# Kernel tuning notes

Measured on AMD Instinct MI355X. Metric: run time of the kernel, lower is better.

Reference implementation:

```python
import jax, jax.numpy as jnp
import numpy as np

N_NODES = 100000
LATENT_DIM = 8
SAMPLE_SIZE = 8192
N_EDGES = 1000000
EPS = 1e-6


def setup_inputs() -> dict:
    key = jax.random.key(0)
    k1, k2, k3, k4, k5 = jax.random.split(key, 5)
    latent_Z = jax.random.normal(k1, (N_NODES, LATENT_DIM), dtype=jnp.float32)
    alpha = jax.random.normal(k2, (1,), dtype=jnp.float32)
    sample_idx = jax.random.randint(k3, (SAMPLE_SIZE,), 0, N_NODES, dtype=jnp.int64)
    sparse_sample_i = jax.random.randint(k4, (N_EDGES,), 0, N_NODES, dtype=jnp.int64)
    sparse_sample_j = jax.random.randint(k5, (N_EDGES,), 0, N_NODES, dtype=jnp.int64)
    return {"latent_Z": latent_Z, "alpha": alpha, "sample_idx": sample_idx,
            "sparse_sample_i": sparse_sample_i, "sparse_sample_j": sparse_sample_j}


def reference(latent_Z, alpha, sample_idx, sparse_sample_i, sparse_sample_j):
    # --- dense non-edge term over the sampled subgraph ---
    Zs = latent_Z[sample_idx]                              # [S, D]
    diff = Zs[:, None, :] - Zs[None, :, :] + EPS           # [S, S, D]
    dist = jnp.sqrt(jnp.sum(diff * diff, axis=-1))         # [S, S]
    mat = jnp.exp(-dist)                                   # [S, S]
    # original uses exp(ones) vectors in the matmul-with-ones trick -> factor e^2
    ones_exp_sq = jnp.exp(jnp.float32(1.0)) ** 2
    offdiag_sum = jnp.sum(mat) - jnp.sum(jnp.diagonal(mat))
    z_pdist1 = jnp.exp(alpha[0]) * 0.5 * ones_exp_sq * offdiag_sum
    # --- sparse positive-edge term ---
    ed = latent_Z[sparse_sample_i] - latent_Z[sparse_sample_j] + EPS  # [E, D]
    edist = jnp.sqrt(jnp.sum(ed * ed, axis=-1))                        # [E]
    z_pdist2 = jnp.sum(-edist + alpha[0])
    return z_pdist2 - z_pdist1
```

## Files before the change

kernel.cpp:

```cpp
#include <hip/hip_runtime.h>
#include <hip/hip_bf16.h>
#include <math.h>

#define NNODES   100000
#define S        8192
#define D        8
#define EPSF     1e-6f
#define LOG2E    1.442695040888963f
#define EPS_S    (LOG2E * EPSF)
#define NT2      256

#define ZHL_OFF  0
#define U_OFF    262144
#define V_OFF    294912
#define DP_OFF   327680
#define SP_OFF   331776
#define ZB_OFF   332800

#define NSBLK    256
#define NDBLK    1024
#define NWPP     32

typedef __attribute__((ext_vector_type(8)))  short short8_t;
typedef __attribute__((ext_vector_type(16))) float f32x16;

__device__ __forceinline__ float block_reduce_f(float v, float* sm) {
    #pragma unroll
    for (int off = 32; off > 0; off >>= 1) v += __shfl_down(v, off, 64);
    int lane = threadIdx.x & 63, wid = threadIdx.x >> 6;
    if (lane == 0) sm[wid] = v;
    __syncthreads();
    float s = 0.f;
    if (threadIdx.x == 0) {
        for (int w = 0; w < 4; ++w) s += sm[w];
    }
    return s;
}

__global__ __launch_bounds__(256) void gather_kernel(const float* __restrict__ Z,
                                                     const int* __restrict__ idx,
                                                     ushort* __restrict__ zhl,
                                                     float* __restrict__ u,
                                                     float* __restrict__ v,
                                                     ushort* __restrict__ zb16) {
    int gid = blockIdx.x * 256 + threadIdx.x;

    if (gid < S) {
        int n = idx[gid];
        const float4* zp = (const float4*)(Z + (size_t)n * D);
        float4 a = zp[0], b = zp[1];
        float z[8] = { a.x, a.y, a.z, a.w, b.x, b.y, b.z, b.w };
        float ss = 0.f;
        short8_t h, l;
        #pragma unroll
        for (int k = 0; k < 8; ++k) {
            float zs = LOG2E * z[k];
            ss = fmaf(zs, zs, ss);
            __hip_bfloat16 hb = __float2bfloat16(zs);
            float hf = __bfloat162float(hb);
            __hip_bfloat16 lb = __float2bfloat16(zs - hf);
            h[k] = (short)__builtin_bit_cast(unsigned short, hb);
            l[k] = (short)__builtin_bit_cast(unsigned short, lb);
        }
        *(short8_t*)(zhl + (size_t)gid * 16)     = h;
        *(short8_t*)(zhl + (size_t)gid * 16 + 8) = l;
        u[gid] = ss + 8.f * EPS_S * EPS_S;
        v[gid] = ss;
    }

    if (gid < NNODES) {
        const float4* zp = (const float4*)(Z + (size_t)gid * D);
        float4 a = zp[0], b = zp[1];
        float z[8] = { a.x, a.y, a.z, a.w, b.x, b.y, b.z, b.w };
        short8_t o;
        #pragma unroll
        for (int k = 0; k < 8; ++k) {
            __hip_bfloat16 bb = __float2bfloat16(z[k]);
            o[k] = (short)__builtin_bit_cast(unsigned short, bb);
        }
        *(short8_t*)(zb16 + (size_t)gid * 8) = o;
    }
}

#define UNPACK8(u4, f)                                        \
    f[0] = __uint_as_float(u4.x << 16);                       \
    f[1] = __uint_as_float(u4.x & 0xffff0000u);               \
    f[2] = __uint_as_float(u4.y << 16);                       \
    f[3] = __uint_as_float(u4.y & 0xffff0000u);               \
    f[4] = __uint_as_float(u4.z << 16);                       \
    f[5] = __uint_as_float(u4.z & 0xffff0000u);               \
    f[6] = __uint_as_float(u4.w << 16);                       \
    f[7] = __uint_as_float(u4.w & 0xffff0000u);

__device__ __forceinline__ float edge_dist4(const uint4* __restrict__ zb,
                                            int4 ia, int4 ib) {
    float acc = 0.f;
    int aidx[4] = { ia.x, ia.y, ia.z, ia.w };
    int bidx[4] = { ib.x, ib.y, ib.z, ib.w };
    #pragma unroll
    for (int q = 0; q < 4; ++q) {
        uint4 ua = zb[aidx[q]];
        uint4 ub = zb[bidx[q]];
        float fa[8], fb[8];
        UNPACK8(ua, fa);
        UNPACK8(ub, fb);
        float s2 = 0.f;
        #pragma unroll
        for (int k = 0; k < 8; ++k) {
            float d = fa[k] - fb[k] + EPSF;
            s2 = fmaf(d, d, s2);
        }
        acc += __builtin_amdgcn_sqrtf(s2);
    }
    return acc;
}

__device__ __forceinline__ void dense_sweep32(const ushort* __restrict__ zhl,
                                              const float* __restrict__ v,
                                              short8_t afrag, const float4* u4,
                                              int ti, int tj0, int cnt, int c31,
                                              float& ax, float& ay, float& az, float& aw) {
    const ushort* bp = zhl + (size_t)(tj0 * 32 + c31) * 16;
    const float*  vp = v + tj0 * 32 + c31;
    short8_t bh = *(const short8_t*)bp;
    short8_t bl = *(const short8_t*)(bp + 8);
    float    vt = vp[0];
    #pragma unroll 2
    for (int t = 0; t < cnt; ++t) {
        short8_t bhc = bh, blc = bl;
        float    vtc = vt;
        if (t + 1 < cnt) {
            bh = *(const short8_t*)(bp + (size_t)(t + 1) * 512);
            bl = *(const short8_t*)(bp + (size_t)(t + 1) * 512 + 8);
            vt = vp[(t + 1) * 32];
        }
        float w = (tj0 + t == ti) ? 1.f : 2.f;
        f32x16 c = { 0.f, 0.f, 0.f, 0.f, 0.f, 0.f, 0.f, 0.f,
                     0.f, 0.f, 0.f, 0.f, 0.f, 0.f, 0.f, 0.f };
        c = __builtin_amdgcn_mfma_f32_32x32x16_bf16(afrag, bhc, c, 0, 0, 0);
        c = __builtin_amdgcn_mfma_f32_32x32x16_bf16(afrag, blc, c, 0, 0, 0);
        #pragma unroll
        for (int q = 0; q < 4; ++q) {
            float s0 = u4[q].x + vtc, s1 = u4[q].y + vtc;
            float s2 = u4[q].z + vtc, s3 = u4[q].w + vtc;
            float d0 = fmaf(c[4*q+0], -2.f, s0);
            float d1 = fmaf(c[4*q+1], -2.f, s1);
            float d2 = fmaf(c[4*q+2], -2.f, s2);
            float d3 = fmaf(c[4*q+3], -2.f, s3);
            ax = fmaf(w, __builtin_amdgcn_exp2f(-__builtin_amdgcn_sqrtf(__builtin_fabsf(d0))), ax);
            ay = fmaf(w, __builtin_amdgcn_exp2f(-__builtin_amdgcn_sqrtf(__builtin_fabsf(d1))), ay);
            az = fmaf(w, __builtin_amdgcn_exp2f(-__builtin_amdgcn_sqrtf(__builtin_fabsf(d2))), az);
            aw = fmaf(w, __builtin_amdgcn_exp2f(-__builtin_amdgcn_sqrtf(__builtin_fabsf(d3))), aw);
        }
    }
}

__global__ __launch_bounds__(256) void fused_kernel(
        const ushort* __restrict__ zhl, const float* __restrict__ u,
        const float* __restrict__ v, const ushort* __restrict__ zb16,
        const int* __restrict__ ei, const int* __restrict__ ej, int ne,
        float* __restrict__ dpart, float* __restrict__ spart) {
    __shared__ float red[4];
    int tid = threadIdx.x, bx = blockIdx.x;

    if (bx < NSBLK) {
        const uint4* zb = (const uint4*)zb16;
        float acc = 0.f;
        int nchunk = ne >> 2;
        int stride = NSBLK * 256;
        int c = bx * 256 + tid;
        if (c < nchunk) {
            int4 ia = ((const int4*)ei)[c];
            int4 ib = ((const int4*)ej)[c];
            while (true) {
                int cn = c + stride;
                int4 ian, ibn;
                bool more = cn < nchunk;
                if (more) {
                    ian = ((const int4*)ei)[cn];
                    ibn = ((const int4*)ej)[cn];
                }
                acc += edge_dist4(zb, ia, ib);
                if (!more) break;
                ia = ian; ib = ibn; c = cn;
            }
        }
        for (int e = (nchunk << 2) + bx * 256 + tid; e < ne; e += stride) {
            uint4 ua = zb[ei[e]];
            uint4 ub = zb[ej[e]];
            float fa[8], fb[8];
            UNPACK8(ua, fa);
            UNPACK8(ub, fb);
            float s2 = 0.f;
            #pragma unroll
            for (int k = 0; k < 8; ++k) {
                float d = fa[k] - fb[k] + EPSF;
                s2 = fmaf(d, d, s2);
            }
            acc += __builtin_amdgcn_sqrtf(s2);
        }
        float s = block_reduce_f(acc, red);
        if (tid == 0) spart[bx] = s;
        return;
    }

    int dbx  = bx - NSBLK;
    int wave = tid >> 6, lane = tid & 63;
    int g = lane >> 5, c31 = lane & 31;

    int p  = dbx >> 3;
    int wv = (dbx & 7) * 4 + wave;
    int k0 = (wv * 257) / NWPP;
    int k1 = ((wv + 1) * 257) / NWPP;
    int n1 = NT2 - p;

    float ax = 0.f, ay = 0.f, az = 0.f, aw = 0.f;

    int eA = k1 < n1 ? k1 : n1;
    if (k0 < eA) {
        int ti = p;
        short8_t afrag = *(const short8_t*)(zhl + (size_t)(ti * 32 + c31) * 16 + g * 8);
        float4 u4[4];
        #pragma unroll
        for (int q = 0; q < 4; ++q) u4[q] = *(const float4*)(u + ti * 32 + 8 * q + 4 * g);
        dense_sweep32(zhl, v, afrag, u4, ti, p + k0, eA - k0, c31, ax, ay, az, aw);
    }
    int sB = k0 > n1 ? k0 : n1;
    if (sB < k1) {
        int ti = (NT2 - 1) - p;
        short8_t afrag = *(const short8_t*)(zhl + (size_t)(ti * 32 + c31) * 16 + g * 8);
        float4 u4[4];
        #pragma unroll
        for (int q = 0; q < 4; ++q) u4[q] = *(const float4*)(u + ti * 32 + 8 * q + 4 * g);
        dense_sweep32(zhl, v, afrag, u4, ti, ti + (sB - n1), k1 - sB, c31, ax, ay, az, aw);
    }
    float s = block_reduce_f((ax + ay) + (az + aw), red);
    if (tid == 0) dpart[dbx] = s;
}

__global__ __launch_bounds__(256) void final_kernel(const float* __restrict__ alpha,
                                                    const float* __restrict__ dpart,
                                                    const float* __restrict__ spart,
                                                    float* __restrict__ out,
                                                    int ne) {
    __shared__ double rd[4], rs[4];
    double ds = 0.0, ss = 0.0;
    for (int k = threadIdx.x; k < NDBLK; k += 256) ds += (double)dpart[k];
    for (int k = threadIdx.x; k < NSBLK; k += 256) ss += (double)spart[k];
    #pragma unroll
    for (int off = 32; off > 0; off >>= 1) {
        ds += __shfl_down(ds, off, 64);
        ss += __shfl_down(ss, off, 64);
    }
    int lane = threadIdx.x & 63, wid = threadIdx.x >> 6;
    if (lane == 0) { rd[wid] = ds; rs[wid] = ss; }
    __syncthreads();
    if (threadIdx.x == 0) {
        double Dsum = 0.0, Ssum = 0.0;
        for (int w = 0; w < 4; ++w) { Dsum += rd[w]; Ssum += rs[w]; }
        double trace = (double)S * exp(-sqrt(8.0) * (double)EPSF);
        double offdiag = Dsum - trace;
        double a = (double)alpha[0];
        double z_pdist2 = (double)ne * a - Ssum;
        double z_pdist1 = exp(a) * 0.5 * 7.3890560989306495 * offdiag;
        out[0] = (float)(z_pdist2 - z_pdist1);
    }
}

extern "C" void kernel_launch(void* const* d_in, const int* in_sizes, int n_in,
                              void* d_out, int out_size, void* d_ws, size_t ws_size,
                              hipStream_t stream) {
    const float* latent_Z = (const float*)d_in[0];
    const float* alpha    = (const float*)d_in[1];
    const int*   sidx     = (const int*)d_in[2];
    const int*   ei       = (const int*)d_in[3];
    const int*   ej       = (const int*)d_in[4];
    int ne = in_sizes[3];
    float* out = (float*)d_out;
    char*  ws  = (char*)d_ws;

    ushort* zhl   = (ushort*)(ws + ZHL_OFF);
    float*  u     = (float*)(ws + U_OFF);
    float*  v     = (float*)(ws + V_OFF);
    float*  dpart = (float*)(ws + DP_OFF);
    float*  spart = (float*)(ws + SP_OFF);
    ushort* zb16  = (ushort*)(ws + ZB_OFF);

    gather_kernel<<<(NNODES + 255) / 256, 256, 0, stream>>>(latent_Z, sidx,
                                                            zhl, u, v, zb16);
    fused_kernel<<<NSBLK + NDBLK, 256, 0, stream>>>(zhl, u, v, zb16, ei, ej, ne,
                                                    dpart, spart);
    final_kernel<<<1, 256, 0, stream>>>(alpha, dpart, spart, out, ne);
}
```

Measured before the change: 30.21 us.

## Fuse final reduction into main kernel via atomic buckets and last-block completion

Removes the separate final reduction kernel. Each block atomically adds its partial sum into one of several padded double buckets, then counts completions through two-level counters, and the last block to finish reads the buckets and writes the output. Bucket and counter zeroing moves into the gather kernel. This is meant to cut one kernel launch and its dependency gap, at the cost of global atomics and fences at block exit, plus a nondeterministic summation order.

```diff
diff --git a/kernel.cpp b/kernel.cpp
--- a/kernel.cpp
+++ b/kernel.cpp
@@ -13,9 +13,9 @@
 #define ZHL_OFF  0
 #define U_OFF    262144
 #define V_OFF    294912
-#define DP_OFF   327680
-#define SP_OFF   331776
-#define ZB_OFF   332800
+#define ZB_OFF   327680
+#define BK_OFF   1928192
+#define NBUCK_BYTES (161 * 128)
 
 #define NSBLK    256
 #define NDBLK    1024
@@ -42,8 +42,13 @@
                                                      ushort* __restrict__ zhl,
                                                      float* __restrict__ u,
                                                      float* __restrict__ v,
-                                                     ushort* __restrict__ zb16) {
+                                                     ushort* __restrict__ zb16,
+                                                     char* __restrict__ buckets) {
     int gid = blockIdx.x * 256 + threadIdx.x;
+
+    if (blockIdx.x == 0 && threadIdx.x < 161) {
+        *(double*)(buckets + threadIdx.x * 128) = 0.0;
+    }
 
     if (gid < S) {
         int n = idx[gid];
@@ -159,9 +164,12 @@
         const ushort* __restrict__ zhl, const float* __restrict__ u,
         const float* __restrict__ v, const ushort* __restrict__ zb16,
         const int* __restrict__ ei, const int* __restrict__ ej, int ne,
-        float* __restrict__ dpart, float* __restrict__ spart) {
+        const float* __restrict__ alpha, char* __restrict__ buckets,
+        float* __restrict__ out) {
     __shared__ float red[4];
+    __shared__ unsigned composeFlag;
     int tid = threadIdx.x, bx = blockIdx.x;
+    float s;
 
     if (bx < NSBLK) {
         const uint4* zb = (const uint4*)zb16;
@@ -199,71 +207,83 @@
             }
             acc += __builtin_amdgcn_sqrtf(s2);
         }
-        float s = block_reduce_f(acc, red);
-        if (tid == 0) spart[bx] = s;
-        return;
-    }
-
-    int dbx  = bx - NSBLK;
-    int wave = tid >> 6, lane = tid & 63;
-    int g = lane >> 5, c31 = lane & 31;
-
-    int p  = dbx >> 3;
-    int wv = (dbx & 7) * 4 + wave;
-    int k0 = (wv * 257) / NWPP;
-    int k1 = ((wv + 1) * 257) / NWPP;
-    int n1 = NT2 - p;
-
-    float ax = 0.f, ay = 0.f, az = 0.f, aw = 0.f;
-
-    int eA = k1 < n1 ? k1 : n1;
-    if (k0 < eA) {
-        int ti = p;
-        short8_t afrag = *(const short8_t*)(zhl + (size_t)(ti * 32 + c31) * 16 + g * 8);
-        float4 u4[4];
-        #pragma unroll
-        for (int q = 0; q < 4; ++q) u4[q] = *(const float4*)(u + ti * 32 + 8 * q + 4 * g);
-        dense_sweep32(zhl, v, afrag, u4, ti, p + k0, eA - k0, c31, ax, ay, az, aw);
-    }
-    int sB = k0 > n1 ? k0 : n1;
-    if (sB < k1) {
-        int ti = (NT2 - 1) - p;
-        short8_t afrag = *(const short8_t*)(zhl + (size_t)(ti * 32 + c31) * 16 + g * 8);
-        float4 u4[4];
-        #pragma unroll
-        for (int q = 0; q < 4; ++q) u4[q] = *(const float4*)(u + ti * 32 + 8 * q + 4 * g);
-        dense_sweep32(zhl, v, afrag, u4, ti, ti + (sB - n1), k1 - sB, c31, ax, ay, az, aw);
-    }
-    float s = block_reduce_f((ax + ay) + (az + aw), red);
-    if (tid == 0) dpart[dbx] = s;
-}
-
-__global__ __launch_bounds__(256) void final_kernel(const float* __restrict__ alpha,
-                                                    const float* __restrict__ dpart,
-                                                    const float* __restrict__ spart,
-                                                    float* __restrict__ out,
-                                                    int ne) {
-    __shared__ double rd[4], rs[4];
-    double ds = 0.0, ss = 0.0;
-    for (int k = threadIdx.x; k < NDBLK; k += 256) ds += (double)dpart[k];
-    for (int k = threadIdx.x; k < NSBLK; k += 256) ss += (double)spart[k];
-    #pragma unroll
-    for (int off = 32; off > 0; off >>= 1) {
-        ds += __shfl_down(ds, off, 64);
-        ss += __shfl_down(ss, off, 64);
-    }
-    int lane = threadIdx.x & 63, wid = threadIdx.x >> 6;
-    if (lane == 0) { rd[wid] = ds; rs[wid] = ss; }
+        s = block_reduce_f(acc, red);
+    } else {
+        int dbx  = bx - NSBLK;
+        int wave = tid >> 6, lane = tid & 63;
+        int g = lane >> 5, c31 = lane & 31;
+
+        int p  = dbx >> 3;
+        int wv = (dbx & 7) * 4 + wave;
+        int k0 = (wv * 257) / NWPP;
+        int k1 = ((wv + 1) * 257) / NWPP;
+        int n1 = NT2 - p;
+
+        float ax = 0.f, ay = 0.f, az = 0.f, aw = 0.f;
+
+        int eA = k1 < n1 ? k1 : n1;
+        if (k0 < eA) {
+            int ti = p;
+            short8_t afrag = *(const short8_t*)(zhl + (size_t)(ti * 32 + c31) * 16 + g * 8);
+            float4 u4[4];
+            #pragma unroll
+            for (int q = 0; q < 4; ++q) u4[q] = *(const float4*)(u + ti * 32 + 8 * q + 4 * g);
+            dense_sweep32(zhl, v, afrag, u4, ti, p + k0, eA - k0, c31, ax, ay, az, aw);
+        }
+        int sB = k0 > n1 ? k0 : n1;
+        if (sB < k1) {
+            int ti = (NT2 - 1) - p;
+            short8_t afrag = *(const short8_t*)(zhl + (size_t)(ti * 32 + c31) * 16 + g * 8);
+            float4 u4[4];
+            #pragma unroll
+            for (int q = 0; q < 4; ++q) u4[q] = *(const float4*)(u + ti * 32 + 8 * q + 4 * g);
+            dense_sweep32(zhl, v, afrag, u4, ti, ti + (sB - n1), k1 - sB, c31, ax, ay, az, aw);
+        }
+        s = block_reduce_f((ax + ay) + (az + aw), red);
+    }
+
+    double* dbuck = (double*)(buckets);
+    double* sbuck = (double*)(buckets + 64 * 128);
+    unsigned* gdone = (unsigned*)(buckets + 160 * 128);
+
+    if (tid == 0) {
+        int  sparse = (bx < NSBLK);
+        int  sid = sparse ? (bx & 15) : ((bx - NSBLK) & 63);
+        int  cid = sparse ? (64 + (bx >> 4)) : ((bx - NSBLK) >> 4);
+        double* sumslot = sparse ? (double*)((char*)sbuck + sid * 128)
+                                 : (double*)((char*)dbuck + sid * 128);
+        (void)atomicAdd(sumslot, (double)s);
+        __builtin_amdgcn_s_waitcnt(0);
+        unsigned oc = atomicAdd((unsigned*)(buckets + (80 + cid) * 128), 1u);
+        unsigned g = 0xFFFFu;
+        if (oc == 15u) {
+            __builtin_amdgcn_s_waitcnt(0);
+            g = atomicAdd(gdone, 1u);
+        }
+        composeFlag = (g == 79u) ? 1u : 0u;
+    }
     __syncthreads();
-    if (threadIdx.x == 0) {
-        double Dsum = 0.0, Ssum = 0.0;
-        for (int w = 0; w < 4; ++w) { Dsum += rd[w]; Ssum += rs[w]; }
-        double trace = (double)S * exp(-sqrt(8.0) * (double)EPSF);
-        double offdiag = Dsum - trace;
-        double a = (double)alpha[0];
-        double z_pdist2 = (double)ne * a - Ssum;
-        double z_pdist1 = exp(a) * 0.5 * 7.3890560989306495 * offdiag;
-        out[0] = (float)(z_pdist2 - z_pdist1);
+
+    if (composeFlag) {
+        __shared__ double acc2[2];
+        int lane = tid & 63, w = tid >> 6;
+        double val = 0.0;
+        if (w == 0) val = atomicAdd((double*)((char*)dbuck + lane * 128), 0.0);
+        else if (w == 1 && lane < 16) val = atomicAdd((double*)((char*)sbuck + lane * 128), 0.0);
+        #pragma unroll
+        for (int off = 32; off > 0; off >>= 1) val += __shfl_down(val, off, 64);
+        if (w == 0 && lane == 0) acc2[0] = val;
+        if (w == 1 && lane == 0) acc2[1] = val;
+        __syncthreads();
+        if (tid == 0) {
+            double Dsum = acc2[0], Ssum = acc2[1];
+            double trace = (double)S * exp(-sqrt(8.0) * (double)EPSF);
+            double offdiag = Dsum - trace;
+            double a = (double)alpha[0];
+            double z_pdist2 = (double)ne * a - Ssum;
+            double z_pdist1 = exp(a) * 0.5 * 7.3890560989306495 * offdiag;
+            out[0] = (float)(z_pdist2 - z_pdist1);
+        }
     }
 }
 
@@ -282,13 +302,11 @@
     ushort* zhl   = (ushort*)(ws + ZHL_OFF);
     float*  u     = (float*)(ws + U_OFF);
     float*  v     = (float*)(ws + V_OFF);
-    float*  dpart = (float*)(ws + DP_OFF);
-    float*  spart = (float*)(ws + SP_OFF);
     ushort* zb16  = (ushort*)(ws + ZB_OFF);
+    char*   bk    = ws + BK_OFF;
 
     gather_kernel<<<(NNODES + 255) / 256, 256, 0, stream>>>(latent_Z, sidx,
-                                                            zhl, u, v, zb16);
+                                                            zhl, u, v, zb16, bk);
     fused_kernel<<<NSBLK + NDBLK, 256, 0, stream>>>(zhl, u, v, zb16, ei, ej, ne,
-                                                    dpart, spart);
-    final_kernel<<<1, 256, 0, stream>>>(alpha, dpart, spart, out, ne);
-}
+                                                    alpha, bk, out);
+}
```

Measured after the change: 30.00 us. About the same (-0.7%).
